# Kernel optimization log

Hardware: AMD Instinct MI355X
Metric: run time of the kernel (lower is better)

Reference implementation:

```python
import jax, jax.numpy as jnp
import numpy as np

S, B, DI, DH, NH = 1024, 64, 256, 256, 4  # seq_len, batch, input_dim, hidden_dim, attn_heads


def _lin(k, fan_in, shape):
    bound = 1.0 / np.sqrt(fan_in)
    return jax.random.uniform(k, shape, jnp.float32, -bound, bound)


def setup_inputs() -> dict:
    key = jax.random.key(0)
    ks = jax.random.split(key, 14)
    inp = {"inputs": jax.random.normal(ks[0], (S, B, DI), jnp.float32)}
    names = ["Wf", "bf", "Wi", "bi", "Wg", "bg", "Wo", "bo"]
    for j in range(4):
        inp[names[2 * j]] = _lin(ks[1 + 2 * j], DI + DH, (DI + DH, DH))
        inp[names[2 * j + 1]] = _lin(ks[2 + 2 * j], DI + DH, (DH,))
    inp["in_proj_w"] = _lin(ks[9], DH, (DH, 3 * DH))
    inp["in_proj_b"] = jnp.zeros((3 * DH,), jnp.float32)
    inp["out_proj_w"] = _lin(ks[10], DH, (DH, DH))
    inp["out_proj_b"] = jnp.zeros((DH,), jnp.float32)
    return inp


def reference(inputs, Wf, bf, Wi, bi, Wg, bg, Wo, bo,
              in_proj_w, in_proj_b, out_proj_w, out_proj_b):
    D = Wf.shape[1]
    bsz = inputs.shape[1]

    def step(carry, x):
        hx, cx = carry
        comb = jnp.concatenate([x, hx], axis=-1)  # [B, DI+DH]
        f = jax.nn.sigmoid(comb @ Wf + bf)
        i = jax.nn.sigmoid(comb @ Wi + bi)
        g = jnp.tanh(comb @ Wg + bg)
        o = jax.nn.sigmoid(comb @ Wo + bo)
        cx = f * cx + i * g
        hx = o * jnp.tanh(cx)
        return (hx, cx), hx

    init = (jnp.zeros((bsz, D), inputs.dtype), jnp.zeros((bsz, D), inputs.dtype))
    (hx, cx), Hseq = jax.lax.scan(step, init, inputs)  # Hseq: [S, B, D]

    # Faithful quirk: nn.MultiheadAttention(batch_first=True) is fed the
    # time-major [S, B, D] tensor, so S acts as the batch dim and attention
    # runs over the B (batch) axis.
    dh = D // NH
    qkv = Hseq @ in_proj_w + in_proj_b  # [S, B, 3D]
    q, k, v = jnp.split(qkv, 3, axis=-1)
    q = q.reshape(S_, bsz, NH, dh) if False else q.reshape(q.shape[0], bsz, NH, dh)
    k = k.reshape(k.shape[0], bsz, NH, dh)
    v = v.reshape(v.shape[0], bsz, NH, dh)
    scale = float(1.0 / np.sqrt(dh))
    scores = jnp.einsum('sqhd,skhd->shqk', q, k) * scale  # [S, H, B, B]
    attn = jax.nn.softmax(scores, axis=-1)
    ctx = jnp.einsum('shqk,skhd->sqhd', attn, v).reshape(Hseq.shape)
    attn_out = ctx @ out_proj_w + out_proj_b
    fused = Hseq + attn_out
    return (fused, (hx, cx))
```

## Files before the change

### kernel.cpp

```cpp
#include <hip/hip_runtime.h>
#include <cstdint>
#include <cstddef>


typedef _Float16 f16;
typedef __attribute__((ext_vector_type(2))) _Float16 half2v;
typedef __attribute__((ext_vector_type(4))) _Float16 half4v;
typedef __attribute__((ext_vector_type(8))) _Float16 half8v;
typedef __attribute__((ext_vector_type(4))) float   float4v;

static __device__ __forceinline__ half2v u2h(unsigned u) {
  union { unsigned u; half2v h; } x; x.u = u; return x.h;
}
static __device__ __forceinline__ float sigm(float x) {
  return 1.0f / (1.0f + __expf(-x));
}
static __device__ __forceinline__ float tanh_fast(float x) {
  x = fminf(15.0f, fmaxf(-15.0f, x));
  float e = __expf(2.0f * x);
  return (e - 1.0f) / (e + 1.0f);
}
static __device__ __forceinline__ const float* selW(int g, const float* a, const float* b,
                                                    const float* c, const float* d) {
  return g == 0 ? a : (g == 1 ? b : (g == 2 ? c : d));
}

__global__ void prep_k(const float* __restrict__ Wf, const float* __restrict__ Wi,
                       const float* __restrict__ Wg_, const float* __restrict__ Wo,
                       const float* __restrict__ bf, const float* __restrict__ bi,
                       const float* __restrict__ bg_, const float* __restrict__ bo,
                       const float* __restrict__ inpw, const float* __restrict__ outpw,
                       f16* __restrict__ wscan, f16* __restrict__ wxt,
                       f16* __restrict__ inpj, f16* __restrict__ outpj,
                       float* __restrict__ bias4)
{
  const int total = 262144 + 262144 + 196608 + 65536 + 1024;
  for (int e = blockIdx.x * blockDim.x + threadIdx.x; e < total; e += gridDim.x * blockDim.x) {
    int x = e;
    if (x < 262144) {
      int c = x >> 8, k = x & 255;
      int g = c >> 8, j = c & 255;
      const float* W = selW(g, Wf, Wi, Wg_, Wo);
      wscan[x] = (f16)W[(256 + k) * 256 + j];
      continue;
    }
    x -= 262144;
    if (x < 262144) {
      int j = x & 7, lane = (x >> 3) & 63, kstep = (x >> 9) & 7, ntile = x >> 12;
      int n = ntile * 16 + (lane & 15);
      int k = kstep * 32 + ((lane >> 4) & 3) * 8 + j;
      int g = n >> 8, jj = n & 255;
      const float* W = selW(g, Wf, Wi, Wg_, Wo);
      wxt[x] = (f16)W[k * 256 + jj];
      continue;
    }
    x -= 262144;
    if (x < 196608) {
      int j = x & 7, lane = (x >> 3) & 63, kstep = (x >> 9) & 7, ntile = x >> 12;
      int n = ntile * 16 + (lane & 15);
      int k = kstep * 32 + ((lane >> 4) & 3) * 8 + j;
      inpj[x] = (f16)inpw[k * 768 + n];
      continue;
    }
    x -= 196608;
    if (x < 65536) {
      int j = x & 7, lane = (x >> 3) & 63, kstep = (x >> 9) & 7, ntile = x >> 12;
      int n = ntile * 16 + (lane & 15);
      int k = kstep * 32 + ((lane >> 4) & 3) * 8 + j;
      outpj[x] = (f16)outpw[k * 256 + n];
      continue;
    }
    x -= 65536;
    {
      int g = x >> 8, j = x & 255;
      const float* bp = selW(g, bf, bi, bg_, bo);
      bias4[x] = bp[j];
    }
  }
}

__global__ void cvt_x_k(const float4v* __restrict__ X, half4v* __restrict__ Xh)
{
  int i = blockIdx.x * 256 + threadIdx.x;
  float4v v = X[i];
  half4v h;
  h.x = (f16)v.x; h.y = (f16)v.y; h.z = (f16)v.z; h.w = (f16)v.w;
  Xh[i] = h;
}

template<int NTOT, bool OUT_EPI>
__global__ __launch_bounds__(256, 2) void gemm_k(const f16* __restrict__ A,
    const f16* __restrict__ Bf, const float* __restrict__ bias,
    f16* __restrict__ Oh, float* __restrict__ Of)
{
  __shared__ f16 Al[8192];
  const int tid = threadIdx.x;
  const int lane = tid & 63;
  const int wm = (tid >> 7) & 1;
  const int wn = (tid >> 6) & 1;
  const int m0 = blockIdx.y * 128, n0 = blockIdx.x * 128;

  float4v acc[4][4];
  #pragma unroll
  for (int i = 0; i < 4; ++i)
    #pragma unroll
    for (int j = 0; j < 4; ++j) { acc[i][j].x = 0.f; acc[i][j].y = 0.f; acc[i][j].z = 0.f; acc[i][j].w = 0.f; }

  #pragma unroll 1
  for (int kc = 0; kc < 4; ++kc) {
    __syncthreads();
    #pragma unroll
    for (int p = 0; p < 4; ++p) {
      int m = p * 32 + (tid >> 3);
      int kk = (tid & 7) * 8;
      half8v v = *(const half8v*)(A + (size_t)(m0 + m) * 256 + kc * 64 + kk);
      int lt = ((kk >> 3) & 3) * 16 + (m & 15);
      *(half8v*)(Al + (((m >> 4) * 2 + (kk >> 5)) * 64 + lt) * 8) = v;
    }
    __syncthreads();
    half8v bfr[4][2], afr[4][2];
    #pragma unroll
    for (int i = 0; i < 4; ++i) {
      int NT = (n0 >> 4) + wn * 4 + i;
      #pragma unroll
      for (int ks = 0; ks < 2; ++ks)
        bfr[i][ks] = *(const half8v*)(Bf + (size_t)((NT * 8 + kc * 2 + ks) * 64 + lane) * 8);
    }
    #pragma unroll
    for (int i = 0; i < 4; ++i) {
      int MT = wm * 4 + i;
      #pragma unroll
      for (int ks = 0; ks < 2; ++ks)
        afr[i][ks] = *(const half8v*)(Al + ((MT * 2 + ks) * 64 + lane) * 8);
    }
    #pragma unroll
    for (int ks = 0; ks < 2; ++ks)
      #pragma unroll
      for (int i = 0; i < 4; ++i)
        #pragma unroll
        for (int jn = 0; jn < 4; ++jn)
          acc[i][jn] = __builtin_amdgcn_mfma_f32_16x16x32_f16(afr[i][ks], bfr[jn][ks], acc[i][jn], 0, 0, 0);
  }

  const int r0 = (lane >> 4) * 4, cn = lane & 15;
  #pragma unroll
  for (int i = 0; i < 4; ++i) {
    #pragma unroll
    for (int jn = 0; jn < 4; ++jn) {
      int n = n0 + wn * 64 + jn * 16 + cn;
      float bv = bias[n];
      int mb = m0 + wm * 64 + i * 16 + r0;
      #pragma unroll
      for (int r = 0; r < 4; ++r) {
        float v = acc[i][jn][r] + bv;
        size_t off = (size_t)(mb + r) * NTOT + n;
        if constexpr (OUT_EPI) Of[off] = v + Of[off];
        else                   Oh[off] = (f16)v;
      }
    }
  }
}

__global__ __launch_bounds__(512, 2) void scan_k(const f16* __restrict__ Xp,
    const f16* __restrict__ Wscan, float* __restrict__ dout, f16* __restrict__ Hh)
{
  extern __shared__ unsigned smem[];
  unsigned* wtl = smem;
  f16* hxs = (f16*)(smem + 32768);
  float* gts = (float*)(smem + 32768 + 128);
  const int tid = threadIdx.x;
  const int b = blockIdx.x;
  const int c0 = tid << 1;
  const unsigned* W32 = (const unsigned*)Wscan;

  unsigned wv[192];
  #pragma unroll
  for (int r = 0; r < 96; ++r) {
    wv[r]      = W32[c0 * 128 + r];
    wv[96 + r] = W32[(c0 + 1) * 128 + r];
  }
  for (int e = tid; e < 32768; e += 512) {
    int r2 = e >> 10, c = e & 1023;
    wtl[(r2 << 10) + c] = W32[c * 128 + 96 + r2];
  }
  if (tid < 128) ((unsigned*)hxs)[tid] = 0u;
  float cx = 0.0f, hx_keep = 0.0f;
  const int gate = tid >> 7;
  __syncthreads();

  #pragma unroll 1
  for (int t = 0; t < 1024; ++t) {
    unsigned xp = ((const unsigned*)Xp)[(size_t)(t * 64 + b) * 512 + tid];
    float a0 = 0.0f, a1 = 0.0f;
    #pragma unroll
    for (int ch = 0; ch < 24; ++ch) {
      half8v h8 = *(const half8v*)(hxs + ch * 8);
      const half2v* hp = (const half2v*)&h8;
      #pragma unroll
      for (int z = 0; z < 4; ++z) {
        int r = ch * 4 + z;
        a0 = __builtin_amdgcn_fdot2(hp[z], u2h(wv[r]), a0, false);
        a1 = __builtin_amdgcn_fdot2(hp[z], u2h(wv[96 + r]), a1, false);
      }
    }
    #pragma unroll
    for (int ch = 0; ch < 8; ++ch) {
      half8v h8 = *(const half8v*)(hxs + 192 + ch * 8);
      const half2v* hp = (const half2v*)&h8;
      #pragma unroll
      for (int z = 0; z < 4; ++z) {
        int r2 = ch * 4 + z;
        uint2 ww = *(const uint2*)(wtl + (r2 << 10) + c0);
        a0 = __builtin_amdgcn_fdot2(hp[z], u2h(ww.x), a0, false);
        a1 = __builtin_amdgcn_fdot2(hp[z], u2h(ww.y), a1, false);
      }
    }
    half2v xph = u2h(xp);
    float p0 = a0 + (float)xph.x;
    float p1 = a1 + (float)xph.y;
    float v0, v1;
    if (gate == 2) { v0 = tanh_fast(p0); v1 = tanh_fast(p1); }
    else           { v0 = sigm(p0);      v1 = sigm(p1); }
    gts[c0] = v0; gts[c0 + 1] = v1;
    __syncthreads();
    if (tid < 256) {
      float fg = gts[tid], ig = gts[256 + tid], gg = gts[512 + tid], og = gts[768 + tid];
      cx = fg * cx + ig * gg;
      float hv = og * tanh_fast(cx);
      hx_keep = hv;
      hxs[tid] = (f16)hv;
      size_t off = (size_t)(t * 64 + b) * 256 + tid;
      dout[off] = hv;
      Hh[off] = (f16)hv;
    }
    __syncthreads();
  }
  if (tid < 256) {
    dout[(size_t)16777216 + b * 256 + tid] = hx_keep;
    dout[(size_t)16777216 + 16384 + b * 256 + tid] = cx;
  }
}

__global__ __launch_bounds__(256, 2) void attn_k(const f16* __restrict__ qkv,
                                                 f16* __restrict__ ctx)
{
  __shared__ f16 ql[64 * 72];
  __shared__ f16 kl[64 * 72];
  __shared__ f16 vT[64 * 72];
  __shared__ f16 at[64 * 72];
  __shared__ float sc[64 * 69];
  __shared__ float pmx[256], psm[256], rmx[64], rsm[64];
  const int tid = threadIdx.x;
  const int s = blockIdx.x >> 2, h = blockIdx.x & 3;
  {
    const int bb = tid >> 2, i = tid & 3;
    const f16* base = qkv + (size_t)(s * 64 + bb) * 768 + h * 64 + i * 16;
    half8v q0 = *(const half8v*)(base);
    half8v q1 = *(const half8v*)(base + 8);
    *(half8v*)(ql + bb * 72 + i * 16)     = q0;
    *(half8v*)(ql + bb * 72 + i * 16 + 8) = q1;
    half8v k0 = *(const half8v*)(base + 256);
    half8v k1 = *(const half8v*)(base + 264);
    *(half8v*)(kl + bb * 72 + i * 16)     = k0;
    *(half8v*)(kl + bb * 72 + i * 16 + 8) = k1;
    half8v v0 = *(const half8v*)(base + 512);
    half8v v1 = *(const half8v*)(base + 520);
    #pragma unroll
    for (int z = 0; z < 8; ++z) {
      vT[(i * 16 + z) * 72 + bb]     = v0[z];
      vT[(i * 16 + 8 + z) * 72 + bb] = v1[z];
    }
  }
  __syncthreads();
  {
    const int qb = tid >> 2, g = tid & 3;
    half8v qr[8];
    #pragma unroll
    for (int i = 0; i < 8; ++i) qr[i] = *(const half8v*)(ql + qb * 72 + i * 8);
    #pragma unroll 1
    for (int jj = 0; jj < 16; ++jj) {
      int kb = g + jj * 4;
      float a = 0.0f;
      #pragma unroll
      for (int i = 0; i < 8; ++i) {
        half8v kr = *(const half8v*)(kl + kb * 72 + i * 8);
        const half2v* kp = (const half2v*)&kr;
        const half2v* qp = (const half2v*)&qr[i];
        #pragma unroll
        for (int z = 0; z < 4; ++z) a = __builtin_amdgcn_fdot2(qp[z], kp[z], a, false);
      }
      sc[qb * 69 + kb] = a * 0.125f;
    }
  }
  __syncthreads();
  {
    const int r = tid & 63, q = tid >> 6;
    float m = -1e30f;
    #pragma unroll
    for (int z = 0; z < 16; ++z) m = fmaxf(m, sc[r * 69 + q * 16 + z]);
    pmx[q * 64 + r] = m;
  }
  __syncthreads();
  if (tid < 64)
    rmx[tid] = fmaxf(fmaxf(pmx[tid], pmx[64 + tid]), fmaxf(pmx[128 + tid], pmx[192 + tid]));
  __syncthreads();
  {
    const int r = tid & 63, q = tid >> 6;
    float mx = rmx[r], ssum = 0.0f;
    #pragma unroll
    for (int z = 0; z < 16; ++z) {
      float e = __expf(sc[r * 69 + q * 16 + z] - mx);
      ssum += e;
      at[r * 72 + q * 16 + z] = (f16)e;
    }
    psm[q * 64 + r] = ssum;
  }
  __syncthreads();
  if (tid < 64)
    rsm[tid] = (psm[tid] + psm[64 + tid]) + (psm[128 + tid] + psm[192 + tid]);
  __syncthreads();
  {
    const int qb = tid >> 2, g = tid & 3;
    half8v ar[8];
    #pragma unroll
    for (int i = 0; i < 8; ++i) ar[i] = *(const half8v*)(at + qb * 72 + i * 8);
    const float rinv = 1.0f / rsm[qb];
    f16* outp = ctx + (size_t)(s * 64 + qb) * 256 + h * 64;
    #pragma unroll 1
    for (int z = 0; z < 16; ++z) {
      int d = g + z * 4;
      float a = 0.0f;
      #pragma unroll
      for (int i = 0; i < 8; ++i) {
        half8v vr = *(const half8v*)(vT + d * 72 + i * 8);
        const half2v* vp = (const half2v*)&vr;
        const half2v* ap = (const half2v*)&ar[i];
        #pragma unroll
        for (int zz = 0; zz < 4; ++zz) a = __builtin_amdgcn_fdot2(ap[zz], vp[zz], a, false);
      }
      outp[d] = (f16)(a * rinv);
    }
  }
}

extern "C" void kernel_launch(void* const* d_in, const int* in_sizes, int n_in,
                              void* d_out, int out_size, void* d_ws, size_t ws_size,
                              hipStream_t stream)
{
  (void)in_sizes; (void)n_in; (void)out_size; (void)ws_size;
  const float* X    = (const float*)d_in[0];
  const float* Wf   = (const float*)d_in[1];
  const float* bf   = (const float*)d_in[2];
  const float* Wi   = (const float*)d_in[3];
  const float* bi   = (const float*)d_in[4];
  const float* Wg   = (const float*)d_in[5];
  const float* bg   = (const float*)d_in[6];
  const float* Wo   = (const float*)d_in[7];
  const float* bo   = (const float*)d_in[8];
  const float* inpw = (const float*)d_in[9];
  const float* inpb = (const float*)d_in[10];
  const float* outpw= (const float*)d_in[11];
  const float* outpb= (const float*)d_in[12];

  char* ws = (char*)d_ws;
  f16*   Xp    = (f16*)(ws + 0);
  f16*   qkv   = (f16*)(ws + 0);
  f16*   ctxh  = (f16*)(ws + 100663296);
  f16*   Xh    = (f16*)(ws + 134217728);
  f16*   Hh    = (f16*)(ws + 167772160);
  f16*   wscan = (f16*)(ws + 201326592);
  f16*   wxt   = (f16*)(ws + 201850880);
  f16*   inpj  = (f16*)(ws + 202375168);
  f16*   outpj = (f16*)(ws + 202768384);
  float* bias4 = (float*)(ws + 202899456);
  float* out   = (float*)d_out;

  prep_k<<<1024, 256, 0, stream>>>(Wf, Wi, Wg, Wo, bf, bi, bg, bo, inpw, outpw,
                                   wscan, wxt, inpj, outpj, bias4);
  cvt_x_k<<<16384, 256, 0, stream>>>((const float4v*)X, (half4v*)Xh);
  gemm_k<1024, false><<<dim3(8, 512), 256, 0, stream>>>(Xh, wxt, bias4, Xp, nullptr);
  scan_k<<<64, 512, 135680, stream>>>(Xp, wscan, out, Hh);
  gemm_k<768, false><<<dim3(6, 512), 256, 0, stream>>>(Hh, inpj, inpb, qkv, nullptr);
  attn_k<<<4096, 256, 0, stream>>>(qkv, ctxh);
  gemm_k<256, true><<<dim3(2, 512), 256, 0, stream>>>(ctxh, outpj, outpb, nullptr, out);
}
```

Before: 2.854 ms.

## Restructure LSTM scan so each thread owns all four gates of one unit

The recurrent scan kernel now uses 256 threads per batch row instead of 512. Each thread computes all four gate pre-activations for one hidden unit and updates the cell state directly, so the gate exchange through shared memory and one barrier per step are gone. The hidden state is double-buffered in LDS, and the input-projection GEMM writes its output gate-interleaved per unit so each thread loads it with one 8-byte read. In exchange each thread holds 104 uint4 weight registers at occupancy 1, which raises register pressure and halves the thread-level parallelism in the dot products.

```diff
diff --git a/kernel.cpp b/kernel.cpp
--- a/kernel.cpp
+++ b/kernel.cpp
@@ -38,10 +38,10 @@
   for (int e = blockIdx.x * blockDim.x + threadIdx.x; e < total; e += gridDim.x * blockDim.x) {
     int x = e;
     if (x < 262144) {
-      int c = x >> 8, k = x & 255;
-      int g = c >> 8, j = c & 255;
+      int q = x >> 13, rem = x & 8191, c = rem >> 3, ee = rem & 7;
+      int k = q * 8 + ee, u = c >> 2, g = c & 3;
       const float* W = selW(g, Wf, Wi, Wg_, Wo);
-      wscan[x] = (f16)W[(256 + k) * 256 + j];
+      wscan[x] = (f16)W[(256 + k) * 256 + u];
       continue;
     }
     x -= 262144;
@@ -88,7 +88,7 @@
   Xh[i] = h;
 }
 
-template<int NTOT, bool OUT_EPI>
+template<int NTOT, int EPI>
 __global__ __launch_bounds__(256, 2) void gemm_k(const f16* __restrict__ A,
     const f16* __restrict__ Bf, const float* __restrict__ bias,
     f16* __restrict__ Oh, float* __restrict__ Of)
@@ -149,96 +149,100 @@
     for (int jn = 0; jn < 4; ++jn) {
       int n = n0 + wn * 64 + jn * 16 + cn;
       float bv = bias[n];
+      int col = (EPI == 1) ? ((n & 255) * 4 + (n >> 8)) : n;
       int mb = m0 + wm * 64 + i * 16 + r0;
       #pragma unroll
       for (int r = 0; r < 4; ++r) {
         float v = acc[i][jn][r] + bv;
-        size_t off = (size_t)(mb + r) * NTOT + n;
-        if constexpr (OUT_EPI) Of[off] = v + Of[off];
-        else                   Oh[off] = (f16)v;
+        size_t off = (size_t)(mb + r) * NTOT + col;
+        if constexpr (EPI == 2) Of[off] = v + Of[off];
+        else                    Oh[off] = (f16)v;
       }
     }
   }
 }
 
-__global__ __launch_bounds__(512, 2) void scan_k(const f16* __restrict__ Xp,
-    const f16* __restrict__ Wscan, float* __restrict__ dout, f16* __restrict__ Hh)
-{
-  extern __shared__ unsigned smem[];
-  unsigned* wtl = smem;
-  f16* hxs = (f16*)(smem + 32768);
-  float* gts = (float*)(smem + 32768 + 128);
+#define DOT_CHUNK(HP, W0, W1, W2, W3)                                        \
+  a0 = __builtin_amdgcn_fdot2(HP[0], u2h((W0).x), a0, false);                \
+  a0 = __builtin_amdgcn_fdot2(HP[1], u2h((W0).y), a0, false);                \
+  a0 = __builtin_amdgcn_fdot2(HP[2], u2h((W0).z), a0, false);                \
+  a0 = __builtin_amdgcn_fdot2(HP[3], u2h((W0).w), a0, false);                \
+  a1 = __builtin_amdgcn_fdot2(HP[0], u2h((W1).x), a1, false);                \
+  a1 = __builtin_amdgcn_fdot2(HP[1], u2h((W1).y), a1, false);                \
+  a1 = __builtin_amdgcn_fdot2(HP[2], u2h((W1).z), a1, false);                \
+  a1 = __builtin_amdgcn_fdot2(HP[3], u2h((W1).w), a1, false);                \
+  a2 = __builtin_amdgcn_fdot2(HP[0], u2h((W2).x), a2, false);                \
+  a2 = __builtin_amdgcn_fdot2(HP[1], u2h((W2).y), a2, false);                \
+  a2 = __builtin_amdgcn_fdot2(HP[2], u2h((W2).z), a2, false);                \
+  a2 = __builtin_amdgcn_fdot2(HP[3], u2h((W2).w), a2, false);                \
+  a3 = __builtin_amdgcn_fdot2(HP[0], u2h((W3).x), a3, false);                \
+  a3 = __builtin_amdgcn_fdot2(HP[1], u2h((W3).y), a3, false);                \
+  a3 = __builtin_amdgcn_fdot2(HP[2], u2h((W3).z), a3, false);                \
+  a3 = __builtin_amdgcn_fdot2(HP[3], u2h((W3).w), a3, false);
+
+__global__ __launch_bounds__(256, 1)
+void scan_k(const f16* __restrict__ Xp, const f16* Wscan,
+            float* __restrict__ dout, f16* __restrict__ Hh)
+{
+  extern __shared__ char smem[];
+  uint4* wtl = (uint4*)smem;
+  f16* hxbuf = (f16*)(smem + 98304);
   const int tid = threadIdx.x;
   const int b = blockIdx.x;
-  const int c0 = tid << 1;
-  const unsigned* W32 = (const unsigned*)Wscan;
-
-  unsigned wv[192];
+  const uint4* Wq = (const uint4*)Wscan;
+
+  for (int e = tid; e < 6144; e += 256) {
+    int j = e >> 10, g = (e >> 8) & 3, u = e & 255;
+    wtl[e] = Wq[(26 + j) * 1024 + u * 4 + g];
+  }
+  uint4 wv[4][26];
   #pragma unroll
-  for (int r = 0; r < 96; ++r) {
-    wv[r]      = W32[c0 * 128 + r];
-    wv[96 + r] = W32[(c0 + 1) * 128 + r];
-  }
-  for (int e = tid; e < 32768; e += 512) {
-    int r2 = e >> 10, c = e & 1023;
-    wtl[(r2 << 10) + c] = W32[c * 128 + 96 + r2];
-  }
-  if (tid < 128) ((unsigned*)hxs)[tid] = 0u;
-  float cx = 0.0f, hx_keep = 0.0f;
-  const int gate = tid >> 7;
+  for (int q = 0; q < 26; ++q)
+    #pragma unroll
+    for (int g = 0; g < 4; ++g)
+      wv[g][q] = Wq[q * 1024 + tid * 4 + g];
+
+  hxbuf[tid] = (f16)0.f;
+  float cx = 0.0f, hv = 0.0f;
+  const uint2* Xp64 = (const uint2*)Xp;
   __syncthreads();
 
   #pragma unroll 1
   for (int t = 0; t < 1024; ++t) {
-    unsigned xp = ((const unsigned*)Xp)[(size_t)(t * 64 + b) * 512 + tid];
-    float a0 = 0.0f, a1 = 0.0f;
-    #pragma unroll
-    for (int ch = 0; ch < 24; ++ch) {
-      half8v h8 = *(const half8v*)(hxs + ch * 8);
+    uint2 xp = Xp64[(size_t)(t * 64 + b) * 256 + tid];
+    const f16* hx = hxbuf + (t & 1) * 256;
+    float a0 = 0.f, a1 = 0.f, a2 = 0.f, a3 = 0.f;
+    #pragma unroll
+    for (int q = 0; q < 26; ++q) {
+      half8v h8 = *(const half8v*)(hx + q * 8);
       const half2v* hp = (const half2v*)&h8;
-      #pragma unroll
-      for (int z = 0; z < 4; ++z) {
-        int r = ch * 4 + z;
-        a0 = __builtin_amdgcn_fdot2(hp[z], u2h(wv[r]), a0, false);
-        a1 = __builtin_amdgcn_fdot2(hp[z], u2h(wv[96 + r]), a1, false);
-      }
-    }
-    #pragma unroll
-    for (int ch = 0; ch < 8; ++ch) {
-      half8v h8 = *(const half8v*)(hxs + 192 + ch * 8);
+      DOT_CHUNK(hp, wv[0][q], wv[1][q], wv[2][q], wv[3][q]);
+    }
+    #pragma unroll
+    for (int j = 0; j < 6; ++j) {
+      half8v h8 = *(const half8v*)(hx + 208 + j * 8);
       const half2v* hp = (const half2v*)&h8;
-      #pragma unroll
-      for (int z = 0; z < 4; ++z) {
-        int r2 = ch * 4 + z;
-        uint2 ww = *(const uint2*)(wtl + (r2 << 10) + c0);
-        a0 = __builtin_amdgcn_fdot2(hp[z], u2h(ww.x), a0, false);
-        a1 = __builtin_amdgcn_fdot2(hp[z], u2h(ww.y), a1, false);
-      }
-    }
-    half2v xph = u2h(xp);
-    float p0 = a0 + (float)xph.x;
-    float p1 = a1 + (float)xph.y;
-    float v0, v1;
-    if (gate == 2) { v0 = tanh_fast(p0); v1 = tanh_fast(p1); }
-    else           { v0 = sigm(p0);      v1 = sigm(p1); }
-    gts[c0] = v0; gts[c0 + 1] = v1;
+      uint4 w0 = wtl[(j * 4 + 0) * 256 + tid];
+      uint4 w1 = wtl[(j * 4 + 1) * 256 + tid];
+      uint4 w2 = wtl[(j * 4 + 2) * 256 + tid];
+      uint4 w3 = wtl[(j * 4 + 3) * 256 + tid];
+      DOT_CHUNK(hp, w0, w1, w2, w3);
+    }
+    half2v x01 = u2h(xp.x), x23 = u2h(xp.y);
+    float fg = sigm(a0 + (float)x01.x);
+    float ig = sigm(a1 + (float)x01.y);
+    float gg = tanh_fast(a2 + (float)x23.x);
+    float og = sigm(a3 + (float)x23.y);
+    cx = fg * cx + ig * gg;
+    hv = og * tanh_fast(cx);
+    hxbuf[((t + 1) & 1) * 256 + tid] = (f16)hv;
+    size_t off = (size_t)(t * 64 + b) * 256 + tid;
+    dout[off] = hv;
+    Hh[off] = (f16)hv;
     __syncthreads();
-    if (tid < 256) {
-      float fg = gts[tid], ig = gts[256 + tid], gg = gts[512 + tid], og = gts[768 + tid];
-      cx = fg * cx + ig * gg;
-      float hv = og * tanh_fast(cx);
-      hx_keep = hv;
-      hxs[tid] = (f16)hv;
-      size_t off = (size_t)(t * 64 + b) * 256 + tid;
-      dout[off] = hv;
-      Hh[off] = (f16)hv;
-    }
-    __syncthreads();
-  }
-  if (tid < 256) {
-    dout[(size_t)16777216 + b * 256 + tid] = hx_keep;
-    dout[(size_t)16777216 + 16384 + b * 256 + tid] = cx;
-  }
+  }
+  dout[(size_t)16777216 + b * 256 + tid] = hv;
+  dout[(size_t)16777216 + 16384 + b * 256 + tid] = cx;
 }
 
 __global__ __launch_bounds__(256, 2) void attn_k(const f16* __restrict__ qkv,
@@ -378,9 +382,9 @@
   prep_k<<<1024, 256, 0, stream>>>(Wf, Wi, Wg, Wo, bf, bi, bg, bo, inpw, outpw,
                                    wscan, wxt, inpj, outpj, bias4);
   cvt_x_k<<<16384, 256, 0, stream>>>((const float4v*)X, (half4v*)Xh);
-  gemm_k<1024, false><<<dim3(8, 512), 256, 0, stream>>>(Xh, wxt, bias4, Xp, nullptr);
-  scan_k<<<64, 512, 135680, stream>>>(Xp, wscan, out, Hh);
-  gemm_k<768, false><<<dim3(6, 512), 256, 0, stream>>>(Hh, inpj, inpb, qkv, nullptr);
+  gemm_k<1024, 1><<<dim3(8, 512), 256, 0, stream>>>(Xh, wxt, bias4, Xp, nullptr);
+  scan_k<<<64, 256, 99328, stream>>>(Xp, wscan, out, Hh);
+  gemm_k<768, 0><<<dim3(6, 512), 256, 0, stream>>>(Hh, inpj, inpb, qkv, nullptr);
   attn_k<<<4096, 256, 0, stream>>>(qkv, ctxh);
-  gemm_k<256, true><<<dim3(2, 512), 256, 0, stream>>>(ctxh, outpj, outpb, nullptr, out);
-}
+  gemm_k<256, 2><<<dim3(2, 512), 256, 0, stream>>>(ctxh, outpj, outpb, nullptr, out);
+}
```

After: 3.756 ms. 1.32x slower.
